# Optimization experiments

Measured on AMD Instinct MI355X. Metric: run time of the kernel, lower is better.

Reference implementation:

```python
import jax, jax.numpy as jnp
import numpy as np
import math

V = 1_000_000   # vocabulary / item count
D = 64          # embedding dim
B = 128         # batch
N = 50          # max_len (targets per user)
K = 1024        # noise_ratio
NORM_TERM = math.log(V)   # norm_term='auto' -> log(noise.numel())
LOG_K = math.log(K)


def setup_inputs() -> dict:
    key = jax.random.key(0)
    k1, k2, k3, k4 = jax.random.split(key, 4)
    target = jax.random.randint(k1, (B, N), 0, V)
    inp = jax.random.normal(k2, (B, N, D), dtype=jnp.float32)
    embs = jax.random.normal(k3, (V, D), dtype=jnp.float32) * 0.02
    # per_word=False: one shared draw of K noise item ids (alias-table sample)
    noise_samples = jax.random.randint(k4, (K,), 0, V)
    # uniform noise distribution, clamped + renormalized then logged
    logprob_noise = jnp.full((V,), -math.log(V), dtype=jnp.float32)
    return {"target": target, "input": inp, "embs": embs,
            "noise_samples": noise_samples, "logprob_noise": logprob_noise}


def _bce_with_logits(x, y):
    # numerically stable BCEWithLogitsLoss (reduction='none')
    return jnp.maximum(x, 0.0) - x * y + jnp.log1p(jnp.exp(-jnp.abs(x)))


def reference(target, input, embs, noise_samples, logprob_noise):
    # --- noise log-probs (irregular gathers over huge table) ---
    logit_noise_in_noise = logprob_noise[noise_samples]          # [K]
    logit_target_in_noise = logprob_noise[target]                # [B,N]
    # --- model scores (get_score) ---
    tgt_emb = embs[target]                                        # [B,N,D] gather
    target_score = jnp.einsum('bnd,bnd->bn', input, tgt_emb)      # [B,N]
    noise_emb = embs[noise_samples]                               # [K,D] gather
    noise_score = jnp.einsum('bnd,kd->bnk', input, noise_emb)     # [B,N,K]
    # --- _get_logit: subtract lnZ ---
    logit_target_in_model = target_score - NORM_TERM
    logit_noise_in_model = noise_score - NORM_TERM
    # --- nce_loss ---
    logits = jnp.concatenate([logit_target_in_model[..., None],
                              logit_noise_in_model], axis=-1)     # [B,N,K+1]
    q_logits = jnp.concatenate(
        [logit_target_in_noise[..., None],
         jnp.broadcast_to(logit_noise_in_noise, (B, N, K))], axis=-1)
    x = logits - q_logits - LOG_K                                 # [B,N,K+1]
    labels = jnp.zeros((B, N, K + 1), dtype=x.dtype).at[..., 0].set(1.0)
    loss = _bce_with_logits(x, labels).sum(axis=-1)               # [B,N]
    # reduction='elementwise_mean'
    return loss.mean()
```

## Files before the change

### kernel.cpp

```cpp
#include <hip/hip_runtime.h>
#include <math.h>

#define DIM 64
#define TILE 64

__device__ __forceinline__ float softplus_fast(float z) {
    return fmaxf(z, 0.f) + __logf(1.f + __expf(-fabsf(z)));
}

__global__ __launch_bounds__(256) void nce_main_kernel(
    const float* __restrict__ inp, const float* __restrict__ embs,
    const int* __restrict__ tgt, const int* __restrict__ ns,
    const float* __restrict__ lpn, float cadd, int nColTiles,
    float* __restrict__ partials)
{
    __shared__ float As[DIM][TILE + 4];
    __shared__ float Bs[DIM][TILE + 4];
    __shared__ float cks[TILE];
    __shared__ float red[4];

    int tid = threadIdx.x;
    int rowTile = blockIdx.x / nColTiles;
    int colTile = blockIdx.x % nColTiles;
    int rBase = rowTile * TILE;
    int cBase = colTile * TILE;

    float s = 0.f;

    if (colTile == 0) {
        int r4 = tid >> 2, q = tid & 3;
        int row = rBase + r4;
        int t = tgt[row];
        const float4* er = (const float4*)(embs + (size_t)t * DIM) + q * 4;
        const float4* ir = (const float4*)(inp + (size_t)row * DIM) + q * 4;
        float p = 0.f;
        #pragma unroll
        for (int j = 0; j < 4; ++j) {
            float4 e = er[j]; float4 a = ir[j];
            p += a.x * e.x + a.y * e.y + a.z * e.z + a.w * e.w;
        }
        p += __shfl_xor(p, 1);
        p += __shfl_xor(p, 2);
        if (q == 0) {
            float x0 = p + cadd - lpn[t];
            s += softplus_fast(-x0);
        }
    }

    const float4* Ag4 = (const float4*)(inp + (size_t)rBase * DIM);
    #pragma unroll
    for (int c = 0; c < 4; ++c) {
        int f = c * 256 + tid;
        int row = f >> 4;
        int dq = f & 15;
        float4 v = Ag4[f];
        As[dq*4+0][row] = v.x; As[dq*4+1][row] = v.y;
        As[dq*4+2][row] = v.z; As[dq*4+3][row] = v.w;
    }
    #pragma unroll
    for (int c = 0; c < 4; ++c) {
        int f = c * 256 + tid;
        int col = f >> 4;
        int dq = f & 15;
        int item = ns[cBase + col];
        float4 v = ((const float4*)(embs + (size_t)item * DIM))[dq];
        Bs[dq*4+0][col] = v.x; Bs[dq*4+1][col] = v.y;
        Bs[dq*4+2][col] = v.z; Bs[dq*4+3][col] = v.w;
    }
    if (tid < TILE) cks[tid] = cadd - lpn[ns[cBase + tid]];
    __syncthreads();

    int tx = tid & 15, ty = tid >> 4;
    float acc[4][4] = {};
    #pragma unroll 16
    for (int d = 0; d < DIM; ++d) {
        float4 a = *(const float4*)&As[d][ty * 4];
        float4 b = *(const float4*)&Bs[d][tx * 4];
        float av[4] = {a.x, a.y, a.z, a.w};
        float bv[4] = {b.x, b.y, b.z, b.w};
        #pragma unroll
        for (int i = 0; i < 4; ++i)
            #pragma unroll
            for (int j = 0; j < 4; ++j)
                acc[i][j] = fmaf(av[i], bv[j], acc[i][j]);
    }

    #pragma unroll
    for (int i = 0; i < 4; ++i)
        #pragma unroll
        for (int j = 0; j < 4; ++j)
            s += softplus_fast(acc[i][j] + cks[tx * 4 + j]);

    #pragma unroll
    for (int off = 32; off > 0; off >>= 1) s += __shfl_xor(s, off);
    int wave = tid >> 6, lane = tid & 63;
    if (lane == 0) red[wave] = s;
    __syncthreads();
    if (tid == 0) partials[blockIdx.x] = red[0] + red[1] + red[2] + red[3];
}

__global__ __launch_bounds__(256) void nce_finalize_kernel(
    const float* __restrict__ partials, int n, float invRows, float* __restrict__ out)
{
    int tid = threadIdx.x;
    float s = 0.f;
    for (int i = tid; i < n; i += 256) s += partials[i];
    #pragma unroll
    for (int off = 32; off > 0; off >>= 1) s += __shfl_xor(s, off);
    __shared__ float red[4];
    int wave = tid >> 6, lane = tid & 63;
    if (lane == 0) red[wave] = s;
    __syncthreads();
    if (tid == 0) out[0] = (red[0] + red[1] + red[2] + red[3]) * invRows;
}

extern "C" void kernel_launch(void* const* d_in, const int* in_sizes, int n_in,
                              void* d_out, int out_size, void* d_ws, size_t ws_size,
                              hipStream_t stream) {
    const int*   target = (const int*)d_in[0];
    const float* input  = (const float*)d_in[1];
    const float* embs   = (const float*)d_in[2];
    const int*   ns     = (const int*)d_in[3];
    const float* lpn    = (const float*)d_in[4];
    float* out = (float*)d_out;

    int nRows = in_sizes[0];
    int K     = in_sizes[3];
    long long V = in_sizes[4];
    float NORM = logf((float)V);
    float LOGK = logf((float)K);
    float cadd = -(NORM + LOGK);

    float* ws = (float*)d_ws;
    int nRowTiles = nRows / TILE;
    int nColTiles = K / TILE;
    int nMain = nRowTiles * nColTiles;

    nce_main_kernel<<<nMain, 256, 0, stream>>>(input, embs, target, ns, lpn,
                                               cadd, nColTiles, ws);
    nce_finalize_kernel<<<1, 256, 0, stream>>>(ws, nMain, 1.0f / (float)nRows, out);
}
```

Baseline: 316.2 us.

## Compute noise scores with bf16 MFMA and spread target dot products across blocks

Replaces the FP32 scalar outer-product GEMM with bf16 MFMA 16x16x32 instructions. Operands are converted to bf16 and stored row-major in LDS with padding. Target-score work, previously done entirely by column-tile-0 blocks, is now split so every block computes four target rows in wave 0, balancing the load. Launch bounds add an occupancy hint. bf16 rounding of the inputs and embeddings reduces dot-product precision.

```diff
diff --git a/kernel.cpp b/kernel.cpp
--- a/kernel.cpp
+++ b/kernel.cpp
@@ -3,23 +3,35 @@
 
 #define DIM 64
 #define TILE 64
+#define LDK 72
+
+typedef __attribute__((ext_vector_type(8))) short short8v;
+typedef __attribute__((ext_vector_type(4))) float floatx4;
+
+struct ushort4s { unsigned short x, y, z, w; };
 
 __device__ __forceinline__ float softplus_fast(float z) {
     return fmaxf(z, 0.f) + __logf(1.f + __expf(-fabsf(z)));
 }
 
-__global__ __launch_bounds__(256) void nce_main_kernel(
+__device__ __forceinline__ unsigned short f2bf(float x) {
+    unsigned u = __builtin_bit_cast(unsigned, x);
+    return (unsigned short)((u + 0x7fffu + ((u >> 16) & 1u)) >> 16);
+}
+
+__global__ __launch_bounds__(256, 6) void nce_main_kernel(
     const float* __restrict__ inp, const float* __restrict__ embs,
     const int* __restrict__ tgt, const int* __restrict__ ns,
     const float* __restrict__ lpn, float cadd, int nColTiles,
     float* __restrict__ partials)
 {
-    __shared__ float As[DIM][TILE + 4];
-    __shared__ float Bs[DIM][TILE + 4];
+    __shared__ unsigned short A_lds[TILE * LDK];
+    __shared__ unsigned short B_lds[TILE * LDK];
     __shared__ float cks[TILE];
     __shared__ float red[4];
 
     int tid = threadIdx.x;
+    int wave = tid >> 6, lane = tid & 63;
     int rowTile = blockIdx.x / nColTiles;
     int colTile = blockIdx.x % nColTiles;
     int rBase = rowTile * TILE;
@@ -27,21 +39,17 @@
 
     float s = 0.f;
 
-    if (colTile == 0) {
-        int r4 = tid >> 2, q = tid & 3;
-        int row = rBase + r4;
+    if (wave == 0) {
+        int row = rBase + colTile * 4 + (lane >> 4);
         int t = tgt[row];
-        const float4* er = (const float4*)(embs + (size_t)t * DIM) + q * 4;
-        const float4* ir = (const float4*)(inp + (size_t)row * DIM) + q * 4;
-        float p = 0.f;
-        #pragma unroll
-        for (int j = 0; j < 4; ++j) {
-            float4 e = er[j]; float4 a = ir[j];
-            p += a.x * e.x + a.y * e.y + a.z * e.z + a.w * e.w;
-        }
+        float4 e = ((const float4*)(embs + (size_t)t * DIM))[lane & 15];
+        float4 a = ((const float4*)(inp + (size_t)row * DIM))[lane & 15];
+        float p = a.x * e.x + a.y * e.y + a.z * e.z + a.w * e.w;
         p += __shfl_xor(p, 1);
         p += __shfl_xor(p, 2);
-        if (q == 0) {
+        p += __shfl_xor(p, 4);
+        p += __shfl_xor(p, 8);
+        if ((lane & 15) == 0) {
             float x0 = p + cadd - lpn[t];
             s += softplus_fast(-x0);
         }
@@ -52,48 +60,45 @@
     for (int c = 0; c < 4; ++c) {
         int f = c * 256 + tid;
         int row = f >> 4;
-        int dq = f & 15;
+        int kq = f & 15;
         float4 v = Ag4[f];
-        As[dq*4+0][row] = v.x; As[dq*4+1][row] = v.y;
-        As[dq*4+2][row] = v.z; As[dq*4+3][row] = v.w;
+        ushort4s b = { f2bf(v.x), f2bf(v.y), f2bf(v.z), f2bf(v.w) };
+        *(ushort4s*)&A_lds[row * LDK + kq * 4] = b;
     }
     #pragma unroll
     for (int c = 0; c < 4; ++c) {
         int f = c * 256 + tid;
         int col = f >> 4;
-        int dq = f & 15;
+        int kq = f & 15;
         int item = ns[cBase + col];
-        float4 v = ((const float4*)(embs + (size_t)item * DIM))[dq];
-        Bs[dq*4+0][col] = v.x; Bs[dq*4+1][col] = v.y;
-        Bs[dq*4+2][col] = v.z; Bs[dq*4+3][col] = v.w;
+        float4 v = ((const float4*)(embs + (size_t)item * DIM))[kq];
+        ushort4s b = { f2bf(v.x), f2bf(v.y), f2bf(v.z), f2bf(v.w) };
+        *(ushort4s*)&B_lds[col * LDK + kq * 4] = b;
     }
     if (tid < TILE) cks[tid] = cadd - lpn[ns[cBase + tid]];
     __syncthreads();
 
-    int tx = tid & 15, ty = tid >> 4;
-    float acc[4][4] = {};
-    #pragma unroll 16
-    for (int d = 0; d < DIM; ++d) {
-        float4 a = *(const float4*)&As[d][ty * 4];
-        float4 b = *(const float4*)&Bs[d][tx * 4];
-        float av[4] = {a.x, a.y, a.z, a.w};
-        float bv[4] = {b.x, b.y, b.z, b.w};
+    int ar = wave * 16 + (lane & 15);
+    int ak = (lane >> 4) * 8;
+    short8v a0 = *(const short8v*)&A_lds[ar * LDK + ak];
+    short8v a1 = *(const short8v*)&A_lds[ar * LDK + 32 + ak];
+
+    #pragma unroll
+    for (int cf = 0; cf < 4; ++cf) {
+        int bc = cf * 16 + (lane & 15);
+        short8v b0 = *(const short8v*)&B_lds[bc * LDK + ak];
+        short8v b1 = *(const short8v*)&B_lds[bc * LDK + 32 + ak];
+        floatx4 acc = {0.f, 0.f, 0.f, 0.f};
+        acc = __builtin_amdgcn_mfma_f32_16x16x32_bf16(a0, b0, acc, 0, 0, 0);
+        acc = __builtin_amdgcn_mfma_f32_16x16x32_bf16(a1, b1, acc, 0, 0, 0);
+        float ck = cks[cf * 16 + (lane & 15)];
         #pragma unroll
-        for (int i = 0; i < 4; ++i)
-            #pragma unroll
-            for (int j = 0; j < 4; ++j)
-                acc[i][j] = fmaf(av[i], bv[j], acc[i][j]);
+        for (int j = 0; j < 4; ++j)
+            s += softplus_fast(acc[j] + ck);
     }
 
     #pragma unroll
-    for (int i = 0; i < 4; ++i)
-        #pragma unroll
-        for (int j = 0; j < 4; ++j)
-            s += softplus_fast(acc[i][j] + cks[tx * 4 + j]);
-
-    #pragma unroll
     for (int off = 32; off > 0; off >>= 1) s += __shfl_xor(s, off);
-    int wave = tid >> 6, lane = tid & 63;
     if (lane == 0) red[wave] = s;
     __syncthreads();
     if (tid == 0) partials[blockIdx.x] = red[0] + red[1] + red[2] + red[3];
```

Measured after the change: 299.3 us. 5.4% less time.
